# Optimization experiments

Hardware: AMD Instinct MI355X
Metric: run time of the kernel (lower is better)

The kernel has to match this reference:

```python
import jax, jax.numpy as jnp
import numpy as np

N, E, IN, HID, OUT = 8192, 262144, 3000, 256, 64
EPS = 1e-5


def setup_inputs() -> dict:
    key = jax.random.key(0)
    k = jax.random.split(key, 16)
    s = lambda i, shp, sc: jax.random.normal(k[i], shp, jnp.float32) * sc
    return {
        "feat": s(0, (N, IN), 1.0),
        "feat_a": s(1, (N, IN), 1.0),
        "graph_neigh": jax.random.uniform(k[2], (N, N), jnp.float32),
        "W1": s(3, (IN, HID), (1.0 / IN) ** 0.5),
        "att_src": s(4, (HID,), (1.0 / HID) ** 0.5),
        "att_dst": s(5, (HID,), (1.0 / HID) ** 0.5),
        "W2": s(6, (HID, OUT), (1.0 / HID) ** 0.5),
        "Wd1": s(7, (OUT, HID), (1.0 / OUT) ** 0.5),
        "bd1": jnp.zeros((HID,), jnp.float32),
        "gamma": jnp.ones((HID,), jnp.float32),
        "beta": jnp.zeros((HID,), jnp.float32),
        "Wd2": s(8, (HID, IN), (1.0 / HID) ** 0.5),
        "bd2": jnp.zeros((IN,), jnp.float32),
        "disc_W": s(9, (OUT, OUT), (1.0 / OUT) ** 0.5),
        "disc_b": jnp.zeros((), jnp.float32),
        "edge_index": jax.random.randint(k[10], (2, E), 0, N),
    }


def _gat_conv1(x, W1, att_src, att_dst, src, dst):
    # GATConv, heads=1, concat=False, no self-loops, no bias
    h = x @ W1                                    # [N, HID]
    a_src = h @ att_src                           # [N]
    a_dst = h @ att_dst                           # [N]
    e = jax.nn.leaky_relu(a_src[src] + a_dst[dst], 0.2)   # [E]
    m = jax.ops.segment_max(e, dst, num_segments=N)
    p = jnp.exp(e - m[dst])
    z = jax.ops.segment_sum(p, dst, num_segments=N)
    alpha = p / (z[dst] + 1e-16)                  # segment softmax over in-edges
    return jax.ops.segment_sum(alpha[:, None] * h[src], dst, num_segments=N)


def _encode(x, W1, att_src, att_dst, W2, src, dst):
    h1 = jax.nn.elu(_gat_conv1(x, W1, att_src, att_dst, src, dst))
    # conv2 is invoked with attention=False -> GraphST GATConv returns only lin(x) (heads=1 mean)
    return h1 @ W2


def _decoder(h, Wd1, bd1, gamma, beta, Wd2, bd2):
    z = h @ Wd1 + bd1
    mu = z.mean(0)
    var = z.var(0)  # biased, matches torch BN training normalization
    z = (z - mu) * jax.lax.rsqrt(var + EPS) * gamma + beta
    z = jax.nn.elu(z)
    return z @ Wd2 + bd2


def _readout(h, mask):
    vsum = mask @ h                               # [N, OUT]
    g = vsum / mask.sum(1, keepdims=True)
    g = g / jnp.clip(jnp.linalg.norm(g, axis=1, keepdims=True), 1e-12)
    return jax.nn.sigmoid(g)


def reference(feat, feat_a, graph_neigh, W1, att_src, att_dst, W2, Wd1, bd1,
              gamma, beta, Wd2, bd2, disc_W, disc_b, edge_index):
    src, dst = edge_index[0], edge_index[1]
    h2 = _encode(feat, W1, att_src, att_dst, W2, src, dst)
    h2_a = _encode(feat_a, W1, att_src, att_dst, W2, src, dst)
    h3 = _decoder(h2, Wd1, bd1, gamma, beta, Wd2, bd2)
    g = _readout(h2, graph_neigh)
    g_a = _readout(h2_a, graph_neigh)

    def disc(c, hp, hm):
        sc1 = jnp.einsum('nd,de,ne->n', hp, disc_W, c) + disc_b
        sc2 = jnp.einsum('nd,de,ne->n', hm, disc_W, c) + disc_b
        return jnp.stack([sc1, sc2], axis=1)

    ret = disc(g, h2, h2_a)
    ret_a = disc(g_a, h2_a, h2)
    return (h2, h3, ret, ret_a, h2, h2_a)
```

## Files before the change

kernel.cpp:

```cpp
#include <hip/hip_runtime.h>
#include <hip/hip_bf16.h>
#include <math.h>

constexpr int NN  = 8192;
constexpr int EE  = 262144;
constexpr int IN  = 3000;
constexpr int INP = 3008;
constexpr int HID = 256;
constexpr int OUT = 64;

constexpr long O_H2   = 0;
constexpr long O_H3   = 524288;
constexpr long O_RET  = 25100288;
constexpr long O_RETA = 25116672;
constexpr long O_H2B  = 25133056;
constexpr long O_H2A  = 25657344;

typedef __attribute__((ext_vector_type(8))) short short8v;
typedef __attribute__((ext_vector_type(4))) float f32x4;

__device__ __forceinline__ short f2bf(float f) {
    unsigned u = __float_as_uint(f);
    return (short)((u + 0x7FFF + ((u >> 16) & 1)) >> 16);
}
__device__ __forceinline__ float bf2f(unsigned short u) {
    return __uint_as_float(((unsigned)u) << 16);
}

__global__ void cvt_W1t(const float* __restrict__ W, unsigned short* __restrict__ Wt) {
    int i = blockIdx.x * 256 + threadIdx.x;
    int n = i / INP, k = i % INP;
    Wt[i] = (k < IN) ? (unsigned short)f2bf(W[(long)k * HID + n]) : 0;
}
__global__ void cvt_W2t(const float* __restrict__ W, unsigned short* __restrict__ Wt) {
    int i = blockIdx.x * 256 + threadIdx.x;
    int n = i / HID, k = i % HID;
    Wt[i] = (unsigned short)f2bf(W[(long)k * OUT + n]);
}
__global__ void cvt_Wd1t(const float* __restrict__ W, unsigned short* __restrict__ Wt) {
    int i = blockIdx.x * 256 + threadIdx.x;
    int n = i / OUT, k = i % OUT;
    Wt[i] = (unsigned short)f2bf(W[(long)k * HID + n]);
}
__global__ void cvt_Wd2t(const float* __restrict__ W, unsigned short* __restrict__ Wt) {
    int i = blockIdx.x * 256 + threadIdx.x;
    int n = i / HID, k = i % HID;
    Wt[i] = (n < IN) ? (unsigned short)f2bf(W[(long)k * IN + n]) : 0;
}
__global__ void cvt_f2b(const float* __restrict__ a, unsigned short* __restrict__ b) {
    int i = blockIdx.x * 256 + threadIdx.x;
    b[i] = (unsigned short)f2bf(a[i]);
}

template<int AF32>
__global__ __launch_bounds__(256) void mfma_gemm128(const void* __restrict__ Av,
                                                    const unsigned short* __restrict__ Bt,
                                                    const float* __restrict__ bias,
                                                    float* __restrict__ Cf,
                                                    float* __restrict__ Cpart,
                                                    int M, int N, int lda, int ldb, int aK,
                                                    int tilesPerChunk, int totalTiles) {
    __shared__ unsigned short As[128][72];
    __shared__ unsigned short Bs[128][72];
    int t = threadIdx.x, w = t >> 6, l = t & 63;
    int row0 = blockIdx.y * 128, col0 = blockIdx.x * 128;
    int sr = t >> 1, sh = (t & 1) * 32;
    int wm = (w >> 1) * 64, wn = (w & 1) * 64;
    int fr = l & 15, fq = l >> 4;
    int kbeg = blockIdx.z * tilesPerChunk * 64;
    int ktiles = min(tilesPerChunk, totalTiles - blockIdx.z * tilesPerChunk);

    const float*          Af = (const float*)Av;
    const unsigned short* Ab = (const unsigned short*)Av;
    const unsigned short* Bp = Bt + (long)(col0 + sr) * ldb + sh;

    float4  paf[8];
    short8v pab[4];
    short8v pb[4];

    auto loadA = [&](int k0) {
        if (AF32) {
            const float* Ar = Af + (long)(row0 + sr) * lda + k0 + sh;
            if (k0 + 64 <= aK) {
#pragma unroll
                for (int q = 0; q < 8; ++q) paf[q] = *reinterpret_cast<const float4*>(Ar + q * 4);
            } else {
#pragma unroll
                for (int q = 0; q < 8; ++q) {
                    float4 v;
                    int kb = k0 + sh + q * 4;
                    v.x = (kb + 0 < aK) ? Ar[q * 4 + 0] : 0.f;
                    v.y = (kb + 1 < aK) ? Ar[q * 4 + 1] : 0.f;
                    v.z = (kb + 2 < aK) ? Ar[q * 4 + 2] : 0.f;
                    v.w = (kb + 3 < aK) ? Ar[q * 4 + 3] : 0.f;
                    paf[q] = v;
                }
            }
        } else {
            const unsigned short* Ar = Ab + (long)(row0 + sr) * lda + k0 + sh;
#pragma unroll
            for (int q = 0; q < 4; ++q) pab[q] = *reinterpret_cast<const short8v*>(Ar + q * 8);
        }
    };
    auto loadB = [&](int k0) {
#pragma unroll
        for (int q = 0; q < 4; ++q) pb[q] = *reinterpret_cast<const short8v*>(Bp + k0 + q * 8);
    };

    loadA(kbeg);
    loadB(kbeg);

    f32x4 acc[4][4] = {};
    for (int tt = 0; tt < ktiles; ++tt) {
        if (AF32) {
#pragma unroll
            for (int q = 0; q < 4; ++q) {
                float4 v0 = paf[q * 2], v1 = paf[q * 2 + 1];
                short8v s;
                s[0]=f2bf(v0.x); s[1]=f2bf(v0.y); s[2]=f2bf(v0.z); s[3]=f2bf(v0.w);
                s[4]=f2bf(v1.x); s[5]=f2bf(v1.y); s[6]=f2bf(v1.z); s[7]=f2bf(v1.w);
                *reinterpret_cast<short8v*>(&As[sr][sh + q * 8]) = s;
            }
        } else {
#pragma unroll
            for (int q = 0; q < 4; ++q)
                *reinterpret_cast<short8v*>(&As[sr][sh + q * 8]) = pab[q];
        }
#pragma unroll
        for (int q = 0; q < 4; ++q)
            *reinterpret_cast<short8v*>(&Bs[sr][sh + q * 8]) = pb[q];
        __syncthreads();
        if (tt + 1 < ktiles) {
            int k0 = kbeg + (tt + 1) * 64;
            loadA(k0);
            loadB(k0);
        }
#pragma unroll
        for (int kk = 0; kk < 2; ++kk) {
            short8v fa[4], fb[4];
#pragma unroll
            for (int i = 0; i < 4; ++i)
                fa[i] = *reinterpret_cast<const short8v*>(&As[wm + i * 16 + fr][kk * 32 + fq * 8]);
#pragma unroll
            for (int j = 0; j < 4; ++j)
                fb[j] = *reinterpret_cast<const short8v*>(&Bs[wn + j * 16 + fr][kk * 32 + fq * 8]);
#pragma unroll
            for (int i = 0; i < 4; ++i)
#pragma unroll
                for (int j = 0; j < 4; ++j)
                    acc[i][j] = __builtin_amdgcn_mfma_f32_16x16x32_bf16(fa[i], fb[j], acc[i][j], 0, 0, 0);
        }
        __syncthreads();
    }
    int dc = l & 15;
#pragma unroll
    for (int i = 0; i < 4; ++i)
#pragma unroll
        for (int j = 0; j < 4; ++j) {
            int c = col0 + wn + j * 16 + dc;
            if (Cpart) {
#pragma unroll
                for (int q = 0; q < 4; ++q) {
                    int r = row0 + wm + i * 16 + fq * 4 + q;
                    Cpart[((long)blockIdx.z * M + r) * N + c] = acc[i][j][q];
                }
            } else if (c < N) {
                float bb = bias ? bias[c] : 0.f;
#pragma unroll
                for (int q = 0; q < 4; ++q) {
                    int r = row0 + wm + i * 16 + fq * 4 + q;
                    Cf[(long)r * N + c] = acc[i][j][q] + bb;
                }
            }
        }
}

__global__ void reduce_cvt(const float* __restrict__ p, unsigned short* __restrict__ hb) {
    int i4 = (blockIdx.x * 256 + threadIdx.x) * 4;
    float4 a = *reinterpret_cast<const float4*>(p + i4);
    float4 b = *reinterpret_cast<const float4*>(p + 2097152 + i4);
    ushort4 r;
    r.x = (unsigned short)f2bf(a.x + b.x);
    r.y = (unsigned short)f2bf(a.y + b.y);
    r.z = (unsigned short)f2bf(a.z + b.z);
    r.w = (unsigned short)f2bf(a.w + b.w);
    *reinterpret_cast<ushort4*>(hb + i4) = r;
}

__global__ __launch_bounds__(256) void mfma_gemm_bf(const unsigned short* __restrict__ A,
                                                    const unsigned short* __restrict__ Bt,
                                                    const float* __restrict__ bias,
                                                    float* __restrict__ C,
                                                    unsigned short* __restrict__ Cb,
                                                    int M, int N, int Kp) {
    __shared__ unsigned short As[64][72];
    __shared__ unsigned short Bs[64][72];
    int t = threadIdx.x, w = t >> 6, l = t & 63;
    int row0 = blockIdx.y * 64, col0 = blockIdx.x * 64;
    int srow = t >> 2, scol = (t & 3) * 16;
    const unsigned short* Ap = A  + (long)(row0 + srow) * Kp + scol;
    const unsigned short* Bp = Bt + (long)(col0 + srow) * Kp + scol;
    int wm = (w >> 1) * 32, wn = (w & 1) * 32;
    int fr = l & 15, fq = l >> 4;
    int nk = Kp >> 6;

    short8v a0r, a1r, b0r, b1r;
    a0r = *reinterpret_cast<const short8v*>(Ap);
    a1r = *reinterpret_cast<const short8v*>(Ap + 8);
    b0r = *reinterpret_cast<const short8v*>(Bp);
    b1r = *reinterpret_cast<const short8v*>(Bp + 8);

    f32x4 acc[2][2] = {};
    for (int tt = 0; tt < nk; ++tt) {
        *reinterpret_cast<short8v*>(&As[srow][scol])     = a0r;
        *reinterpret_cast<short8v*>(&As[srow][scol + 8]) = a1r;
        *reinterpret_cast<short8v*>(&Bs[srow][scol])     = b0r;
        *reinterpret_cast<short8v*>(&Bs[srow][scol + 8]) = b1r;
        __syncthreads();
        if (tt + 1 < nk) {
            const unsigned short* Ap2 = Ap + (tt + 1) * 64;
            const unsigned short* Bp2 = Bp + (tt + 1) * 64;
            a0r = *reinterpret_cast<const short8v*>(Ap2);
            a1r = *reinterpret_cast<const short8v*>(Ap2 + 8);
            b0r = *reinterpret_cast<const short8v*>(Bp2);
            b1r = *reinterpret_cast<const short8v*>(Bp2 + 8);
        }
#pragma unroll
        for (int kk = 0; kk < 2; ++kk) {
            short8v fa0 = *reinterpret_cast<const short8v*>(&As[wm + fr][kk * 32 + fq * 8]);
            short8v fa1 = *reinterpret_cast<const short8v*>(&As[wm + 16 + fr][kk * 32 + fq * 8]);
            short8v fb0 = *reinterpret_cast<const short8v*>(&Bs[wn + fr][kk * 32 + fq * 8]);
            short8v fb1 = *reinterpret_cast<const short8v*>(&Bs[wn + 16 + fr][kk * 32 + fq * 8]);
            acc[0][0] = __builtin_amdgcn_mfma_f32_16x16x32_bf16(fa0, fb0, acc[0][0], 0, 0, 0);
            acc[0][1] = __builtin_amdgcn_mfma_f32_16x16x32_bf16(fa0, fb1, acc[0][1], 0, 0, 0);
            acc[1][0] = __builtin_amdgcn_mfma_f32_16x16x32_bf16(fa1, fb0, acc[1][0], 0, 0, 0);
            acc[1][1] = __builtin_amdgcn_mfma_f32_16x16x32_bf16(fa1, fb1, acc[1][1], 0, 0, 0);
        }
        __syncthreads();
    }
    int dc = l & 15;
#pragma unroll
    for (int i = 0; i < 2; ++i)
#pragma unroll
        for (int j = 0; j < 2; ++j) {
            int c = col0 + wn + j * 16 + dc;
            if (c < N) {
                float bb = bias ? bias[c] : 0.f;
#pragma unroll
                for (int q = 0; q < 4; ++q) {
                    int r = row0 + wm + i * 16 + fq * 4 + q;
                    float v = acc[i][j][q] + bb;
                    long idx = (long)r * N + c;
                    if (C)  C[idx]  = v;
                    if (Cb) Cb[idx] = (unsigned short)f2bf(v);
                }
            }
        }
}

__global__ __launch_bounds__(256) void readout_mfma2(const float* __restrict__ gn,
                                                     const unsigned short* __restrict__ HT,
                                                     float* __restrict__ vsum_part,
                                                     float* __restrict__ rowsum_part) {
    __shared__ unsigned short As[64][72];
    __shared__ unsigned short Bs[128][72];
    __shared__ float rsacc[64][4];
    int t = threadIdx.x, w = t >> 6, l = t & 63;
    int row0 = blockIdx.x * 64;
    int kc = blockIdx.y, kbeg = kc * 2048;
    int asr = t >> 2, asc = (t & 3) * 16;
    int bsr = t >> 1, bsc = (t & 1) * 32;
    const float*          Ap = gn + (long)(row0 + asr) * NN + kbeg + asc;
    const unsigned short* Bp = HT + (long)bsr * NN + kbeg + bsc;
    int wm = (w >> 1) * 32, wn = (w & 1) * 64;
    int fr = l & 15, fq = l >> 4;

    float4  a4[4];
    short8v b8[4];
#pragma unroll
    for (int q = 0; q < 4; ++q) a4[q] = *reinterpret_cast<const float4*>(Ap + q * 4);
#pragma unroll
    for (int q = 0; q < 4; ++q) b8[q] = *reinterpret_cast<const short8v*>(Bp + q * 8);

    f32x4 acc[2][4] = {};
    float myrs = 0.f;
    for (int it = 0; it < 32; ++it) {
#pragma unroll
        for (int q = 0; q < 4; ++q) {
            float4 v = a4[q];
            ushort4 s;
            s.x = (unsigned short)f2bf(v.x);
            s.y = (unsigned short)f2bf(v.y);
            s.z = (unsigned short)f2bf(v.z);
            s.w = (unsigned short)f2bf(v.w);
            *reinterpret_cast<ushort4*>(&As[asr][asc + q * 4]) = s;
            myrs += v.x + v.y + v.z + v.w;
        }
#pragma unroll
        for (int q = 0; q < 4; ++q)
            *reinterpret_cast<short8v*>(&Bs[bsr][bsc + q * 8]) = b8[q];
        __syncthreads();
        if (it + 1 < 32) {
            const float*          Ap2 = Ap + (it + 1) * 64;
            const unsigned short* Bp2 = Bp + (it + 1) * 64;
#pragma unroll
            for (int q = 0; q < 4; ++q) a4[q] = *reinterpret_cast<const float4*>(Ap2 + q * 4);
#pragma unroll
            for (int q = 0; q < 4; ++q) b8[q] = *reinterpret_cast<const short8v*>(Bp2 + q * 8);
        }
#pragma unroll
        for (int kk = 0; kk < 2; ++kk) {
            short8v fa0 = *reinterpret_cast<const short8v*>(&As[wm + fr][kk * 32 + fq * 8]);
            short8v fa1 = *reinterpret_cast<const short8v*>(&As[wm + 16 + fr][kk * 32 + fq * 8]);
#pragma unroll
            for (int j = 0; j < 4; ++j) {
                short8v fb = *reinterpret_cast<const short8v*>(&Bs[wn + j * 16 + fr][kk * 32 + fq * 8]);
                acc[0][j] = __builtin_amdgcn_mfma_f32_16x16x32_bf16(fa0, fb, acc[0][j], 0, 0, 0);
                acc[1][j] = __builtin_amdgcn_mfma_f32_16x16x32_bf16(fa1, fb, acc[1][j], 0, 0, 0);
            }
        }
        __syncthreads();
    }
    rsacc[asr][t & 3] = myrs;
    __syncthreads();
    if (t < 64)
        rowsum_part[(long)kc * NN + row0 + t] =
            rsacc[t][0] + rsacc[t][1] + rsacc[t][2] + rsacc[t][3];
    int dc = l & 15;
#pragma unroll
    for (int i = 0; i < 2; ++i)
#pragma unroll
        for (int j = 0; j < 4; ++j) {
            int c = wn + j * 16 + dc;
#pragma unroll
            for (int q = 0; q < 4; ++q) {
                int r = row0 + wm + i * 16 + fq * 4 + q;
                vsum_part[((long)kc * NN + r) * 128 + c] = acc[i][j][q];
            }
        }
}

__global__ void deg_count(const int* __restrict__ dst, int* __restrict__ deg) {
    int i = blockIdx.x * 256 + threadIdx.x;
    if (i < EE) atomicAdd(&deg[dst[i]], 1);
}

__global__ __launch_bounds__(256) void scan_offsets(const int* __restrict__ deg,
                                                    int* __restrict__ off,
                                                    int* __restrict__ cursor) {
    __shared__ int part[256];
    int t = threadIdx.x;
    int base = t * 32;
    int local[32];
    int s = 0;
#pragma unroll
    for (int i = 0; i < 32; ++i) { local[i] = s; s += deg[base + i]; }
    part[t] = s;
    __syncthreads();
    for (int o2 = 1; o2 < 256; o2 <<= 1) {
        int v = (t >= o2) ? part[t - o2] : 0;
        __syncthreads();
        part[t] += v;
        __syncthreads();
    }
    int pre = (t == 0) ? 0 : part[t - 1];
#pragma unroll
    for (int i = 0; i < 32; ++i) {
        int v = pre + local[i];
        off[base + i] = v;
        cursor[base + i] = v;
    }
}

__global__ void scatter_edges(const int* __restrict__ src, const int* __restrict__ dst,
                              int* __restrict__ cursor, int* __restrict__ ssrc) {
    int i = blockIdx.x * 256 + threadIdx.x;
    if (i >= EE) return;
    int slot = atomicAdd(&cursor[dst[i]], 1);
    ssrc[slot] = src[i];
}

__global__ void attn_coeff_bf(const unsigned short* __restrict__ h,
                              const float* __restrict__ att_src,
                              const float* __restrict__ att_dst,
                              float* __restrict__ a_src, float* __restrict__ a_dst) {
    int wave = threadIdx.x >> 6, lane = threadIdx.x & 63;
    int n = blockIdx.x * 4 + wave;
    ushort4 hv = *reinterpret_cast<const ushort4*>(&h[(long)n * HID + lane * 4]);
    float4 vs = *reinterpret_cast<const float4*>(&att_src[lane * 4]);
    float4 vd = *reinterpret_cast<const float4*>(&att_dst[lane * 4]);
    float h0 = bf2f(hv.x), h1 = bf2f(hv.y), h2v = bf2f(hv.z), h3v = bf2f(hv.w);
    float s1 = h0 * vs.x + h1 * vs.y + h2v * vs.z + h3v * vs.w;
    float s2 = h0 * vd.x + h1 * vd.y + h2v * vd.z + h3v * vd.w;
#pragma unroll
    for (int off = 32; off > 0; off >>= 1) {
        s1 += __shfl_down(s1, off);
        s2 += __shfl_down(s2, off);
    }
    if (lane == 0) { a_src[n] = s1; a_dst[n] = s2; }
}

__global__ __launch_bounds__(256) void gat_gather(const int* __restrict__ ssrc,
                                                  const int* __restrict__ off,
                                                  const int* __restrict__ deg,
                                                  const float* __restrict__ asrc,
                                                  const float* __restrict__ adst,
                                                  const unsigned short* __restrict__ h,
                                                  unsigned short* __restrict__ gat) {
    int wv = threadIdx.x >> 6, lane = threadIdx.x & 63;
    int d = blockIdx.x * 4 + wv;
    int o = off[d], n = deg[d];
    float ad = adst[d];

    float m = -INFINITY;
    for (int j = lane; j < n; j += 64) {
        float e = asrc[ssrc[o + j]] + ad;
        e = e > 0.f ? e : 0.2f * e;
        m = fmaxf(m, e);
    }
#pragma unroll
    for (int t = 32; t; t >>= 1) m = fmaxf(m, __shfl_xor(m, t));
    float z = 0.f;
    for (int j = lane; j < n; j += 64) {
        float e = asrc[ssrc[o + j]] + ad;
        e = e > 0.f ? e : 0.2f * e;
        z += expf(e - m);
    }
#pragma unroll
    for (int t = 32; t; t >>= 1) z += __shfl_xor(z, t);
    float zinv = 1.0f / (z + 1e-16f);

    float4 acc = {0.f, 0.f, 0.f, 0.f};
    int j = 0;
    for (; j + 2 <= n; j += 2) {
        int s0 = ssrc[o + j], s1 = ssrc[o + j + 1];
        const ushort4 h0 = *reinterpret_cast<const ushort4*>(&h[(long)s0 * HID + lane * 4]);
        const ushort4 h1 = *reinterpret_cast<const ushort4*>(&h[(long)s1 * HID + lane * 4]);
        float e0 = asrc[s0] + ad; e0 = e0 > 0.f ? e0 : 0.2f * e0;
        float e1 = asrc[s1] + ad; e1 = e1 > 0.f ? e1 : 0.2f * e1;
        float a0 = expf(e0 - m) * zinv;
        float a1 = expf(e1 - m) * zinv;
        acc.x += a0 * bf2f(h0.x) + a1 * bf2f(h1.x);
        acc.y += a0 * bf2f(h0.y) + a1 * bf2f(h1.y);
        acc.z += a0 * bf2f(h0.z) + a1 * bf2f(h1.z);
        acc.w += a0 * bf2f(h0.w) + a1 * bf2f(h1.w);
    }
    if (j < n) {
        int s0 = ssrc[o + j];
        const ushort4 h0 = *reinterpret_cast<const ushort4*>(&h[(long)s0 * HID + lane * 4]);
        float e0 = asrc[s0] + ad; e0 = e0 > 0.f ? e0 : 0.2f * e0;
        float a0 = expf(e0 - m) * zinv;
        acc.x += a0 * bf2f(h0.x); acc.y += a0 * bf2f(h0.y);
        acc.z += a0 * bf2f(h0.z); acc.w += a0 * bf2f(h0.w);
    }
    ushort4 r;
    r.x = (unsigned short)f2bf(acc.x > 0.f ? acc.x : expm1f(acc.x));
    r.y = (unsigned short)f2bf(acc.y > 0.f ? acc.y : expm1f(acc.y));
    r.z = (unsigned short)f2bf(acc.z > 0.f ? acc.z : expm1f(acc.z));
    r.w = (unsigned short)f2bf(acc.w > 0.f ? acc.w : expm1f(acc.w));
    *reinterpret_cast<ushort4*>(&gat[(long)d * HID + lane * 4]) = r;
}

__global__ void bn_partial(const float* __restrict__ zd, float* __restrict__ s,
                           float* __restrict__ sq) {
    int t = threadIdx.x;
    float a = 0.f, b = 0.f;
    int r0 = blockIdx.x * 128;
    for (int r = r0; r < r0 + 128; ++r) {
        float v = zd[(long)r * HID + t];
        a += v;
        b += v * v;
    }
    atomicAdd(&s[t], a);
    atomicAdd(&sq[t], b);
}

__global__ void bn_finalize(const float* __restrict__ s, const float* __restrict__ sq,
                            const float* __restrict__ gamma, const float* __restrict__ beta,
                            float* __restrict__ scale, float* __restrict__ shift) {
    int t = threadIdx.x;
    float mean = s[t] / (float)NN;
    float var  = sq[t] / (float)NN - mean * mean;
    float sc   = gamma[t] * rsqrtf(var + 1e-5f);
    scale[t] = sc;
    shift[t] = beta[t] - mean * sc;
}

__global__ void bn_apply_elu_bf(const float* __restrict__ zd, const float* __restrict__ scale,
                                const float* __restrict__ shift, unsigned short* __restrict__ zb) {
    for (long i = (long)blockIdx.x * blockDim.x + threadIdx.x; i < (long)NN * HID;
         i += (long)gridDim.x * blockDim.x) {
        int c = (int)(i & 255);
        float v = zd[i] * scale[c] + shift[c];
        v = v > 0.f ? v : expm1f(v);
        zb[i] = (unsigned short)f2bf(v);
    }
}

__global__ void pack_hcatT(const float* __restrict__ h2, const float* __restrict__ h2a,
                           unsigned short* __restrict__ HT) {
    int c = blockIdx.x;
    int r = blockIdx.y * 256 + threadIdx.x;
    float v = (c < 64) ? h2[(long)r * 64 + c] : h2a[(long)r * 64 + (c - 64)];
    HT[(long)c * NN + r] = (unsigned short)f2bf(v);
}

__global__ void readout_norm2(const float* __restrict__ vsum_part,
                              const float* __restrict__ rowsum_part,
                              float* __restrict__ g, float* __restrict__ ga) {
    int r = blockIdx.x;
    int c = threadIdx.x;
    float v = 0.f;
#pragma unroll
    for (int kc = 0; kc < 4; ++kc)
        v += vsum_part[((long)kc * NN + r) * 128 + c];
    float rs = 0.f;
#pragma unroll
    for (int kc = 0; kc < 4; ++kc)
        rs += rowsum_part[(long)kc * NN + r];
    v /= rs;
    int w = c >> 6, lane = c & 63;
    float sq = v * v;
#pragma unroll
    for (int off = 32; off > 0; off >>= 1) sq += __shfl_xor(sq, off);
    float nrm = fmaxf(sqrtf(sq), 1e-12f);
    float out = 1.0f / (1.0f + expf(-(v / nrm)));
    (w == 0 ? g : ga)[(long)r * 64 + lane] = out;
}

__global__ void disc_kernel(const float* __restrict__ h2, const float* __restrict__ h2a,
                            const float* __restrict__ g, const float* __restrict__ ga,
                            const float* __restrict__ W, const float* __restrict__ b,
                            float* __restrict__ ret, float* __restrict__ reta) {
    int n = blockIdx.x;
    int w = threadIdx.x >> 6, lane = threadIdx.x & 63;
    const float* c = (w == 0) ? g : ga;
    float u = 0.f;
#pragma unroll 8
    for (int e = 0; e < 64; ++e) u += W[lane * 64 + e] * c[(long)n * 64 + e];
    float hp = ((w == 0) ? h2 : h2a)[(long)n * 64 + lane];
    float hm = ((w == 0) ? h2a : h2)[(long)n * 64 + lane];
    float t1 = hp * u, t2 = hm * u;
    for (int off = 32; off > 0; off >>= 1) {
        t1 += __shfl_xor(t1, off);
        t2 += __shfl_xor(t2, off);
    }
    if (lane == 0) {
        float bb = b[0];
        if (w == 0) { ret[n * 2] = t1 + bb;  ret[n * 2 + 1] = t2 + bb; }
        else        { reta[n * 2] = t1 + bb; reta[n * 2 + 1] = t2 + bb; }
    }
}

__global__ void copy_h2(const float* __restrict__ h2, const float* __restrict__ h2a,
                        float* __restrict__ out) {
    int i = blockIdx.x * 256 + threadIdx.x;
    float v = h2[i], va = h2a[i];
    out[O_H2 + i]  = v;
    out[O_H2B + i] = v;
    out[O_H2A + i] = va;
}

extern "C" void kernel_launch(void* const* d_in, const int* in_sizes, int n_in,
                              void* d_out, int out_size, void* d_ws, size_t ws_size,
                              hipStream_t stream) {
    const float* feat    = (const float*)d_in[0];
    const float* feat_a  = (const float*)d_in[1];
    const float* gneigh  = (const float*)d_in[2];
    const float* W1      = (const float*)d_in[3];
    const float* att_src = (const float*)d_in[4];
    const float* att_dst = (const float*)d_in[5];
    const float* W2      = (const float*)d_in[6];
    const float* Wd1     = (const float*)d_in[7];
    const float* bd1     = (const float*)d_in[8];
    const float* gamma   = (const float*)d_in[9];
    const float* beta    = (const float*)d_in[10];
    const float* Wd2     = (const float*)d_in[11];
    const float* bd2     = (const float*)d_in[12];
    const float* disc_W  = (const float*)d_in[13];
    const float* disc_b  = (const float*)d_in[14];
    const int*   eidx    = (const int*)d_in[15];
    const int*   src = eidx;
    const int*   dst = eidx + EE;
    float* out = (float*)d_out;

    float* w = (float*)d_ws;
    float* h_buf   = w;
    unsigned short* h_bf = (unsigned short*)h_buf;
    unsigned short* gat_bf = (unsigned short*)(h_buf + 2097152);
    float* zdec    = h_buf + 2097152 + 1048576;
    unsigned short* zdec_bf = (unsigned short*)(zdec + 2097152);
    float* h2      = zdec + 2097152 + 1048576;
    float* h2a     = h2 + 524288;
    float* gbuf    = h2a + 524288;
    float* gabuf   = gbuf + 524288;
    unsigned short* h2b = (unsigned short*)(gabuf + 524288);
    float* asrc    = gabuf + 524288 + 262144;
    float* adst    = asrc + 8192;
    float* bnsum   = adst + 8192;
    float* bnsq    = bnsum + 256;
    float* scale   = bnsq + 256;
    float* shift   = scale + 256;
    unsigned short* W1t  = (unsigned short*)(shift + 256);
    unsigned short* W2t  = W1t + 770048;
    unsigned short* Wd1t = W2t + 16384;
    unsigned short* Wd2t = Wd1t + 16384;
    int*   ideg    = (int*)(Wd2t + 786432);
    int*   ioff    = ideg + 8192;
    int*   icur    = ioff + 8192;
    int*   issrc   = icur + 8192;
    float* part = w + 2097152;
    float* vsum_part = h_buf;
    unsigned short* HT = zdec_bf;
    float* rowsum_part = ((float*)zdec_bf) + 524288;

    cvt_W1t<<<3008, 256, 0, stream>>>(W1, W1t);
    cvt_W2t<<<64, 256, 0, stream>>>(W2, W2t);
    cvt_Wd1t<<<64, 256, 0, stream>>>(Wd1, Wd1t);
    cvt_Wd2t<<<3072, 256, 0, stream>>>(Wd2, Wd2t);

    hipMemsetAsync(ideg, 0, 8192 * 4, stream);
    deg_count<<<EE / 256, 256, 0, stream>>>(dst, ideg);
    scan_offsets<<<1, 256, 0, stream>>>(ideg, ioff, icur);
    scatter_edges<<<EE / 256, 256, 0, stream>>>(src, dst, icur, issrc);

    auto encode_pass = [&](const float* x, float* h2_out) {
        mfma_gemm128<1><<<dim3(2, 64, 2), 256, 0, stream>>>(
            x, W1t, nullptr, nullptr, part, NN, HID, IN, INP, IN, 24, 47);
        reduce_cvt<<<2048, 256, 0, stream>>>(part, h_bf);
        attn_coeff_bf<<<2048, 256, 0, stream>>>(h_bf, att_src, att_dst, asrc, adst);
        gat_gather<<<2048, 256, 0, stream>>>(issrc, ioff, ideg, asrc, adst, h_bf, gat_bf);
        mfma_gemm_bf<<<dim3(1, 128), 256, 0, stream>>>(gat_bf, W2t, nullptr,
                                                       h2_out, h2b, NN, OUT, HID);
    };

    encode_pass(feat, h2);
    encode_pass(feat_a, h2a);
    cvt_f2b<<<2048, 256, 0, stream>>>(h2, h2b);

    mfma_gemm_bf<<<dim3(4, 128), 256, 0, stream>>>(h2b, Wd1t, bd1,
                                                   zdec, nullptr, NN, HID, OUT);
    hipMemsetAsync(bnsum, 0, 512 * 4, stream);
    bn_partial<<<64, 256, 0, stream>>>(zdec, bnsum, bnsq);
    bn_finalize<<<1, 256, 0, stream>>>(bnsum, bnsq, gamma, beta, scale, shift);
    bn_apply_elu_bf<<<2048, 256, 0, stream>>>(zdec, scale, shift, zdec_bf);
    mfma_gemm128<0><<<dim3(24, 64, 1), 256, 0, stream>>>(
        zdec_bf, Wd2t, bd2, out + O_H3, nullptr, NN, IN, HID, HID, HID, 4, 4);

    pack_hcatT<<<dim3(128, 32), 256, 0, stream>>>(h2, h2a, HT);
    readout_mfma2<<<dim3(128, 4), 256, 0, stream>>>(gneigh, HT, vsum_part, rowsum_part);
    readout_norm2<<<8192, 128, 0, stream>>>(vsum_part, rowsum_part, gbuf, gabuf);

    disc_kernel<<<8192, 128, 0, stream>>>(h2, h2a, gbuf, gabuf, disc_W, disc_b,
                                          out + O_RET, out + O_RETA);

    copy_h2<<<2048, 256, 0, stream>>>(h2, h2a, out);
}
```

Measured before the change: 449.8 us.

## Batch both encoder passes into single launches and fuse epilogues and readout kernels

Both encoder passes (feat and feat_a) now run in one launch each for the W1 GEMM, attention coefficients, GAT gather and W2 GEMM. The split-K partial buffer and its reduce kernel are gone: the W1 GEMM runs over the full K and writes bf16 directly. The W2 GEMM epilogue also writes the fp32 outputs, the bf16 copy and the transposed readout operand, which removes the cvt, pack and copy kernels. Readout normalization and the discriminator are merged into one kernel. This cuts launches and intermediate memory traffic, but the W1 GEMM drops from 256 blocks of 24 K-tiles to 256 blocks of 47 K-tiles, so each block runs a longer serial K loop.

```diff
diff --git a/kernel.cpp b/kernel.cpp
--- a/kernel.cpp
+++ b/kernel.cpp
@@ -47,94 +47,67 @@
     int n = i / HID, k = i % HID;
     Wt[i] = (n < IN) ? (unsigned short)f2bf(W[(long)k * IN + n]) : 0;
 }
-__global__ void cvt_f2b(const float* __restrict__ a, unsigned short* __restrict__ b) {
-    int i = blockIdx.x * 256 + threadIdx.x;
-    b[i] = (unsigned short)f2bf(a[i]);
-}
-
-template<int AF32>
-__global__ __launch_bounds__(256) void mfma_gemm128(const void* __restrict__ Av,
-                                                    const unsigned short* __restrict__ Bt,
-                                                    const float* __restrict__ bias,
-                                                    float* __restrict__ Cf,
-                                                    float* __restrict__ Cpart,
-                                                    int M, int N, int lda, int ldb, int aK,
-                                                    int tilesPerChunk, int totalTiles) {
+
+__global__ __launch_bounds__(256) void feat_gemm(const float* __restrict__ A0,
+                                                 const float* __restrict__ A1,
+                                                 const unsigned short* __restrict__ Bt,
+                                                 unsigned short* __restrict__ Hb) {
     __shared__ unsigned short As[128][72];
     __shared__ unsigned short Bs[128][72];
+    int id = blockIdx.x;
+    int xb = id >> 7, yb = id & 127;
+    int pass = yb >> 6;
+    int row0 = (yb & 63) * 128, col0 = xb * 128;
+    const float* A = pass ? A1 : A0;
     int t = threadIdx.x, w = t >> 6, l = t & 63;
-    int row0 = blockIdx.y * 128, col0 = blockIdx.x * 128;
     int sr = t >> 1, sh = (t & 1) * 32;
     int wm = (w >> 1) * 64, wn = (w & 1) * 64;
     int fr = l & 15, fq = l >> 4;
-    int kbeg = blockIdx.z * tilesPerChunk * 64;
-    int ktiles = min(tilesPerChunk, totalTiles - blockIdx.z * tilesPerChunk);
-
-    const float*          Af = (const float*)Av;
-    const unsigned short* Ab = (const unsigned short*)Av;
-    const unsigned short* Bp = Bt + (long)(col0 + sr) * ldb + sh;
+    const unsigned short* Bp = Bt + (long)(col0 + sr) * INP + sh;
+    const float* Arow = A + (long)(row0 + sr) * IN;
 
     float4  paf[8];
-    short8v pab[4];
     short8v pb[4];
-
     auto loadA = [&](int k0) {
-        if (AF32) {
-            const float* Ar = Af + (long)(row0 + sr) * lda + k0 + sh;
-            if (k0 + 64 <= aK) {
-#pragma unroll
-                for (int q = 0; q < 8; ++q) paf[q] = *reinterpret_cast<const float4*>(Ar + q * 4);
-            } else {
-#pragma unroll
-                for (int q = 0; q < 8; ++q) {
-                    float4 v;
-                    int kb = k0 + sh + q * 4;
-                    v.x = (kb + 0 < aK) ? Ar[q * 4 + 0] : 0.f;
-                    v.y = (kb + 1 < aK) ? Ar[q * 4 + 1] : 0.f;
-                    v.z = (kb + 2 < aK) ? Ar[q * 4 + 2] : 0.f;
-                    v.w = (kb + 3 < aK) ? Ar[q * 4 + 3] : 0.f;
-                    paf[q] = v;
-                }
+        const float* Ar = Arow + k0 + sh;
+        if (k0 + 64 <= IN) {
+#pragma unroll
+            for (int q = 0; q < 8; ++q) paf[q] = *reinterpret_cast<const float4*>(Ar + q * 4);
+        } else {
+#pragma unroll
+            for (int q = 0; q < 8; ++q) {
+                int kb = k0 + sh + q * 4;
+                float4 v;
+                v.x = (kb + 0 < IN) ? Ar[q * 4 + 0] : 0.f;
+                v.y = (kb + 1 < IN) ? Ar[q * 4 + 1] : 0.f;
+                v.z = (kb + 2 < IN) ? Ar[q * 4 + 2] : 0.f;
+                v.w = (kb + 3 < IN) ? Ar[q * 4 + 3] : 0.f;
+                paf[q] = v;
             }
-        } else {
-            const unsigned short* Ar = Ab + (long)(row0 + sr) * lda + k0 + sh;
-#pragma unroll
-            for (int q = 0; q < 4; ++q) pab[q] = *reinterpret_cast<const short8v*>(Ar + q * 8);
         }
     };
     auto loadB = [&](int k0) {
 #pragma unroll
         for (int q = 0; q < 4; ++q) pb[q] = *reinterpret_cast<const short8v*>(Bp + k0 + q * 8);
     };
-
-    loadA(kbeg);
-    loadB(kbeg);
-
+    loadA(0); loadB(0);
+
+    constexpr int NK = INP / 64;
     f32x4 acc[4][4] = {};
-    for (int tt = 0; tt < ktiles; ++tt) {
-        if (AF32) {
-#pragma unroll
-            for (int q = 0; q < 4; ++q) {
-                float4 v0 = paf[q * 2], v1 = paf[q * 2 + 1];
-                short8v s;
-                s[0]=f2bf(v0.x); s[1]=f2bf(v0.y); s[2]=f2bf(v0.z); s[3]=f2bf(v0.w);
-                s[4]=f2bf(v1.x); s[5]=f2bf(v1.y); s[6]=f2bf(v1.z); s[7]=f2bf(v1.w);
-                *reinterpret_cast<short8v*>(&As[sr][sh + q * 8]) = s;
-            }
-        } else {
-#pragma unroll
-            for (int q = 0; q < 4; ++q)
-                *reinterpret_cast<short8v*>(&As[sr][sh + q * 8]) = pab[q];
+    for (int tt = 0; tt < NK; ++tt) {
+#pragma unroll
+        for (int q = 0; q < 4; ++q) {
+            float4 v0 = paf[q * 2], v1 = paf[q * 2 + 1];
+            short8v s;
+            s[0]=f2bf(v0.x); s[1]=f2bf(v0.y); s[2]=f2bf(v0.z); s[3]=f2bf(v0.w);
+            s[4]=f2bf(v1.x); s[5]=f2bf(v1.y); s[6]=f2bf(v1.z); s[7]=f2bf(v1.w);
+            *reinterpret_cast<short8v*>(&As[sr][sh + q * 8]) = s;
         }
 #pragma unroll
         for (int q = 0; q < 4; ++q)
             *reinterpret_cast<short8v*>(&Bs[sr][sh + q * 8]) = pb[q];
         __syncthreads();
-        if (tt + 1 < ktiles) {
-            int k0 = kbeg + (tt + 1) * 64;
-            loadA(k0);
-            loadB(k0);
-        }
+        if (tt + 1 < NK) { loadA((tt + 1) * 64); loadB((tt + 1) * 64); }
 #pragma unroll
         for (int kk = 0; kk < 2; ++kk) {
             short8v fa[4], fb[4];
@@ -153,56 +126,35 @@
         __syncthreads();
     }
     int dc = l & 15;
+    long base = (long)(pass * NN) * HID;
 #pragma unroll
     for (int i = 0; i < 4; ++i)
 #pragma unroll
         for (int j = 0; j < 4; ++j) {
             int c = col0 + wn + j * 16 + dc;
-            if (Cpart) {
-#pragma unroll
-                for (int q = 0; q < 4; ++q) {
-                    int r = row0 + wm + i * 16 + fq * 4 + q;
-                    Cpart[((long)blockIdx.z * M + r) * N + c] = acc[i][j][q];
-                }
-            } else if (c < N) {
-                float bb = bias ? bias[c] : 0.f;
-#pragma unroll
-                for (int q = 0; q < 4; ++q) {
-                    int r = row0 + wm + i * 16 + fq * 4 + q;
-                    Cf[(long)r * N + c] = acc[i][j][q] + bb;
-                }
+#pragma unroll
+            for (int q = 0; q < 4; ++q) {
+                int r = row0 + wm + i * 16 + fq * 4 + q;
+                Hb[base + (long)r * HID + c] = (unsigned short)f2bf(acc[i][j][q]);
             }
         }
 }
 
-__global__ void reduce_cvt(const float* __restrict__ p, unsigned short* __restrict__ hb) {
-    int i4 = (blockIdx.x * 256 + threadIdx.x) * 4;
-    float4 a = *reinterpret_cast<const float4*>(p + i4);
-    float4 b = *reinterpret_cast<const float4*>(p + 2097152 + i4);
-    ushort4 r;
-    r.x = (unsigned short)f2bf(a.x + b.x);
-    r.y = (unsigned short)f2bf(a.y + b.y);
-    r.z = (unsigned short)f2bf(a.z + b.z);
-    r.w = (unsigned short)f2bf(a.w + b.w);
-    *reinterpret_cast<ushort4*>(hb + i4) = r;
-}
-
-__global__ __launch_bounds__(256) void mfma_gemm_bf(const unsigned short* __restrict__ A,
-                                                    const unsigned short* __restrict__ Bt,
-                                                    const float* __restrict__ bias,
-                                                    float* __restrict__ C,
-                                                    unsigned short* __restrict__ Cb,
-                                                    int M, int N, int Kp) {
+__global__ __launch_bounds__(256) void w2_gemm(const unsigned short* __restrict__ A,
+                                               const unsigned short* __restrict__ Bt,
+                                               float* __restrict__ h2f,
+                                               unsigned short* __restrict__ h2b,
+                                               unsigned short* __restrict__ HT,
+                                               float* __restrict__ out) {
     __shared__ unsigned short As[64][72];
     __shared__ unsigned short Bs[64][72];
     int t = threadIdx.x, w = t >> 6, l = t & 63;
-    int row0 = blockIdx.y * 64, col0 = blockIdx.x * 64;
+    int row0 = blockIdx.y * 64;
     int srow = t >> 2, scol = (t & 3) * 16;
-    const unsigned short* Ap = A  + (long)(row0 + srow) * Kp + scol;
-    const unsigned short* Bp = Bt + (long)(col0 + srow) * Kp + scol;
+    const unsigned short* Ap = A + (long)(row0 + srow) * HID + scol;
+    const unsigned short* Bp = Bt + (long)srow * HID + scol;
     int wm = (w >> 1) * 32, wn = (w & 1) * 32;
     int fr = l & 15, fq = l >> 4;
-    int nk = Kp >> 6;
 
     short8v a0r, a1r, b0r, b1r;
     a0r = *reinterpret_cast<const short8v*>(Ap);
@@ -211,13 +163,13 @@
     b1r = *reinterpret_cast<const short8v*>(Bp + 8);
 
     f32x4 acc[2][2] = {};
-    for (int tt = 0; tt < nk; ++tt) {
+    for (int tt = 0; tt < 4; ++tt) {
         *reinterpret_cast<short8v*>(&As[srow][scol])     = a0r;
         *reinterpret_cast<short8v*>(&As[srow][scol + 8]) = a1r;
         *reinterpret_cast<short8v*>(&Bs[srow][scol])     = b0r;
         *reinterpret_cast<short8v*>(&Bs[srow][scol + 8]) = b1r;
         __syncthreads();
-        if (tt + 1 < nk) {
+        if (tt + 1 < 4) {
             const unsigned short* Ap2 = Ap + (tt + 1) * 64;
             const unsigned short* Bp2 = Bp + (tt + 1) * 64;
             a0r = *reinterpret_cast<const short8v*>(Ap2);
@@ -239,21 +191,142 @@
         __syncthreads();
     }
     int dc = l & 15;
+    int pass = row0 >> 13;
+#pragma unroll
+    for (int i = 0; i < 2; ++i)
+#pragma unroll
+        for (int j = 0; j < 2; ++j) {
+            int c = wn + j * 16 + dc;
+#pragma unroll
+            for (int q = 0; q < 4; ++q) {
+                int r = row0 + wm + i * 16 + fq * 4 + q;
+                int n = r & 8191;
+                float v = acc[i][j][q];
+                unsigned short vb = (unsigned short)f2bf(v);
+                h2f[(long)pass * 524288 + (long)n * 64 + c] = v;
+                if (pass == 0) {
+                    out[O_H2  + (long)n * 64 + c] = v;
+                    out[O_H2B + (long)n * 64 + c] = v;
+                    h2b[(long)n * 64 + c] = vb;
+                } else {
+                    out[O_H2A + (long)n * 64 + c] = v;
+                }
+                HT[(long)(pass * 64 + c) * NN + n] = vb;
+            }
+        }
+}
+
+__global__ __launch_bounds__(256) void wd2_gemm(const unsigned short* __restrict__ A,
+                                                const unsigned short* __restrict__ Bt,
+                                                const float* __restrict__ bias,
+                                                float* __restrict__ Cf) {
+    __shared__ unsigned short As[128][72];
+    __shared__ unsigned short Bs[128][72];
+    int t = threadIdx.x, w = t >> 6, l = t & 63;
+    int row0 = blockIdx.y * 128, col0 = blockIdx.x * 128;
+    int sr = t >> 1, sh = (t & 1) * 32;
+    int wm = (w >> 1) * 64, wn = (w & 1) * 64;
+    int fr = l & 15, fq = l >> 4;
+    const unsigned short* Ap = A  + (long)(row0 + sr) * HID + sh;
+    const unsigned short* Bp = Bt + (long)(col0 + sr) * HID + sh;
+
+    short8v pa[4], pb[4];
+#pragma unroll
+    for (int q = 0; q < 4; ++q) pa[q] = *reinterpret_cast<const short8v*>(Ap + q * 8);
+#pragma unroll
+    for (int q = 0; q < 4; ++q) pb[q] = *reinterpret_cast<const short8v*>(Bp + q * 8);
+
+    f32x4 acc[4][4] = {};
+    for (int tt = 0; tt < 4; ++tt) {
+#pragma unroll
+        for (int q = 0; q < 4; ++q) {
+            *reinterpret_cast<short8v*>(&As[sr][sh + q * 8]) = pa[q];
+            *reinterpret_cast<short8v*>(&Bs[sr][sh + q * 8]) = pb[q];
+        }
+        __syncthreads();
+        if (tt + 1 < 4) {
+            int k0 = (tt + 1) * 64;
+#pragma unroll
+            for (int q = 0; q < 4; ++q) pa[q] = *reinterpret_cast<const short8v*>(Ap + k0 + q * 8);
+#pragma unroll
+            for (int q = 0; q < 4; ++q) pb[q] = *reinterpret_cast<const short8v*>(Bp + k0 + q * 8);
+        }
+#pragma unroll
+        for (int kk = 0; kk < 2; ++kk) {
+            short8v fa[4], fb[4];
+#pragma unroll
+            for (int i = 0; i < 4; ++i)
+                fa[i] = *reinterpret_cast<const short8v*>(&As[wm + i * 16 + fr][kk * 32 + fq * 8]);
+#pragma unroll
+            for (int j = 0; j < 4; ++j)
+                fb[j] = *reinterpret_cast<const short8v*>(&Bs[wn + j * 16 + fr][kk * 32 + fq * 8]);
+#pragma unroll
+            for (int i = 0; i < 4; ++i)
+#pragma unroll
+                for (int j = 0; j < 4; ++j)
+                    acc[i][j] = __builtin_amdgcn_mfma_f32_16x16x32_bf16(fa[i], fb[j], acc[i][j], 0, 0, 0);
+        }
+        __syncthreads();
+    }
+    int dc = l & 15;
+#pragma unroll
+    for (int i = 0; i < 4; ++i)
+#pragma unroll
+        for (int j = 0; j < 4; ++j) {
+            int c = col0 + wn + j * 16 + dc;
+            if (c < IN) {
+                float bb = bias[c];
+#pragma unroll
+                for (int q = 0; q < 4; ++q) {
+                    int r = row0 + wm + i * 16 + fq * 4 + q;
+                    Cf[(long)r * IN + c] = acc[i][j][q] + bb;
+                }
+            }
+        }
+}
+
+__global__ __launch_bounds__(256) void wd1_gemm(const unsigned short* __restrict__ A,
+                                                const unsigned short* __restrict__ Bt,
+                                                const float* __restrict__ bias,
+                                                float* __restrict__ C) {
+    __shared__ unsigned short As[64][72];
+    __shared__ unsigned short Bs[64][72];
+    int t = threadIdx.x, w = t >> 6, l = t & 63;
+    int row0 = blockIdx.y * 64, col0 = blockIdx.x * 64;
+    int srow = t >> 2, scol = (t & 3) * 16;
+    const unsigned short* Ap = A  + (long)(row0 + srow) * OUT + scol;
+    const unsigned short* Bp = Bt + (long)(col0 + srow) * OUT + scol;
+    int wm = (w >> 1) * 32, wn = (w & 1) * 32;
+    int fr = l & 15, fq = l >> 4;
+
+    *reinterpret_cast<short8v*>(&As[srow][scol])     = *reinterpret_cast<const short8v*>(Ap);
+    *reinterpret_cast<short8v*>(&As[srow][scol + 8]) = *reinterpret_cast<const short8v*>(Ap + 8);
+    *reinterpret_cast<short8v*>(&Bs[srow][scol])     = *reinterpret_cast<const short8v*>(Bp);
+    *reinterpret_cast<short8v*>(&Bs[srow][scol + 8]) = *reinterpret_cast<const short8v*>(Bp + 8);
+    __syncthreads();
+    f32x4 acc[2][2] = {};
+#pragma unroll
+    for (int kk = 0; kk < 2; ++kk) {
+        short8v fa0 = *reinterpret_cast<const short8v*>(&As[wm + fr][kk * 32 + fq * 8]);
+        short8v fa1 = *reinterpret_cast<const short8v*>(&As[wm + 16 + fr][kk * 32 + fq * 8]);
+        short8v fb0 = *reinterpret_cast<const short8v*>(&Bs[wn + fr][kk * 32 + fq * 8]);
+        short8v fb1 = *reinterpret_cast<const short8v*>(&Bs[wn + 16 + fr][kk * 32 + fq * 8]);
+        acc[0][0] = __builtin_amdgcn_mfma_f32_16x16x32_bf16(fa0, fb0, acc[0][0], 0, 0, 0);
+        acc[0][1] = __builtin_amdgcn_mfma_f32_16x16x32_bf16(fa0, fb1, acc[0][1], 0, 0, 0);
+        acc[1][0] = __builtin_amdgcn_mfma_f32_16x16x32_bf16(fa1, fb0, acc[1][0], 0, 0, 0);
+        acc[1][1] = __builtin_amdgcn_mfma_f32_16x16x32_bf16(fa1, fb1, acc[1][1], 0, 0, 0);
+    }
+    int dc = l & 15;
 #pragma unroll
     for (int i = 0; i < 2; ++i)
 #pragma unroll
         for (int j = 0; j < 2; ++j) {
             int c = col0 + wn + j * 16 + dc;
-            if (c < N) {
-                float bb = bias ? bias[c] : 0.f;
-#pragma unroll
-                for (int q = 0; q < 4; ++q) {
-                    int r = row0 + wm + i * 16 + fq * 4 + q;
-                    float v = acc[i][j][q] + bb;
-                    long idx = (long)r * N + c;
-                    if (C)  C[idx]  = v;
-                    if (Cb) Cb[idx] = (unsigned short)f2bf(v);
-                }
+            float bb = bias[c];
+#pragma unroll
+            for (int q = 0; q < 4; ++q) {
+                int r = row0 + wm + i * 16 + fq * 4 + q;
+                C[(long)r * HID + c] = acc[i][j][q] + bb;
             }
         }
 }
@@ -403,14 +476,17 @@
 __global__ __launch_bounds__(256) void gat_gather(const int* __restrict__ ssrc,
                                                   const int* __restrict__ off,
                                                   const int* __restrict__ deg,
-                                                  const float* __restrict__ asrc,
-                                                  const float* __restrict__ adst,
-                                                  const unsigned short* __restrict__ h,
-                                                  unsigned short* __restrict__ gat) {
+                                                  const float* __restrict__ asrc2,
+                                                  const float* __restrict__ adst2,
+                                                  const unsigned short* __restrict__ hb2,
+                                                  unsigned short* __restrict__ gat2) {
     int wv = threadIdx.x >> 6, lane = threadIdx.x & 63;
     int d = blockIdx.x * 4 + wv;
-    int o = off[d], n = deg[d];
-    float ad = adst[d];
+    int pass = d >> 13, node = d & 8191;
+    const float* asrc = asrc2 + pass * NN;
+    const unsigned short* h = hb2 + (long)pass * NN * HID;
+    int o = off[node], n = deg[node];
+    float ad = adst2[d];
 
     float m = -INFINITY;
     for (int j = lane; j < n; j += 64) {
@@ -458,7 +534,7 @@
     r.y = (unsigned short)f2bf(acc.y > 0.f ? acc.y : expm1f(acc.y));
     r.z = (unsigned short)f2bf(acc.z > 0.f ? acc.z : expm1f(acc.z));
     r.w = (unsigned short)f2bf(acc.w > 0.f ? acc.w : expm1f(acc.w));
-    *reinterpret_cast<ushort4*>(&gat[(long)d * HID + lane * 4]) = r;
+    *reinterpret_cast<ushort4*>(&gat2[(long)d * HID + lane * 4]) = r;
 }
 
 __global__ void bn_partial(const float* __restrict__ zd, float* __restrict__ s,
@@ -497,68 +573,46 @@
     }
 }
 
-__global__ void pack_hcatT(const float* __restrict__ h2, const float* __restrict__ h2a,
-                           unsigned short* __restrict__ HT) {
-    int c = blockIdx.x;
-    int r = blockIdx.y * 256 + threadIdx.x;
-    float v = (c < 64) ? h2[(long)r * 64 + c] : h2a[(long)r * 64 + (c - 64)];
-    HT[(long)c * NN + r] = (unsigned short)f2bf(v);
-}
-
-__global__ void readout_norm2(const float* __restrict__ vsum_part,
-                              const float* __restrict__ rowsum_part,
-                              float* __restrict__ g, float* __restrict__ ga) {
-    int r = blockIdx.x;
-    int c = threadIdx.x;
-    float v = 0.f;
-#pragma unroll
-    for (int kc = 0; kc < 4; ++kc)
-        v += vsum_part[((long)kc * NN + r) * 128 + c];
-    float rs = 0.f;
-#pragma unroll
-    for (int kc = 0; kc < 4; ++kc)
+__global__ void readout_disc(const float* __restrict__ vsum_part,
+                             const float* __restrict__ rowsum_part,
+                             const float* __restrict__ h2f,
+                             const float* __restrict__ W, const float* __restrict__ b,
+                             float* __restrict__ ret, float* __restrict__ reta) {
+    __shared__ float gg[128];
+    int r = blockIdx.x, t = threadIdx.x;
+    float rs = 0.f, v = 0.f;
+#pragma unroll
+    for (int kc = 0; kc < 4; ++kc) {
         rs += rowsum_part[(long)kc * NN + r];
+        v  += vsum_part[((long)kc * NN + r) * 128 + t];
+    }
     v /= rs;
-    int w = c >> 6, lane = c & 63;
+    int w = t >> 6, lane = t & 63;
     float sq = v * v;
 #pragma unroll
     for (int off = 32; off > 0; off >>= 1) sq += __shfl_xor(sq, off);
     float nrm = fmaxf(sqrtf(sq), 1e-12f);
-    float out = 1.0f / (1.0f + expf(-(v / nrm)));
-    (w == 0 ? g : ga)[(long)r * 64 + lane] = out;
-}
-
-__global__ void disc_kernel(const float* __restrict__ h2, const float* __restrict__ h2a,
-                            const float* __restrict__ g, const float* __restrict__ ga,
-                            const float* __restrict__ W, const float* __restrict__ b,
-                            float* __restrict__ ret, float* __restrict__ reta) {
-    int n = blockIdx.x;
-    int w = threadIdx.x >> 6, lane = threadIdx.x & 63;
-    const float* c = (w == 0) ? g : ga;
+    gg[t] = 1.0f / (1.0f + expf(-(v / nrm)));
+    __syncthreads();
+    const float* hp_base = h2f + (w ? 524288 : 0);
+    const float* hm_base = h2f + (w ? 0 : 524288);
     float u = 0.f;
 #pragma unroll 8
-    for (int e = 0; e < 64; ++e) u += W[lane * 64 + e] * c[(long)n * 64 + e];
-    float hp = ((w == 0) ? h2 : h2a)[(long)n * 64 + lane];
-    float hm = ((w == 0) ? h2a : h2)[(long)n * 64 + lane];
+    for (int e = 0; e < 64; ++e) u += W[lane * 64 + e] * gg[w * 64 + e];
+    float hp = hp_base[(long)r * 64 + lane];
+    float hm = hm_base[(long)r * 64 + lane];
     float t1 = hp * u, t2 = hm * u;
+#pragma unroll
     for (int off = 32; off > 0; off >>= 1) {
         t1 += __shfl_xor(t1, off);
         t2 += __shfl_xor(t2, off);
     }
     if (lane == 0) {
         float bb = b[0];
-        if (w == 0) { ret[n * 2] = t1 + bb;  ret[n * 2 + 1] = t2 + bb; }
-        else        { reta[n * 2] = t1 + bb; reta[n * 2 + 1] = t2 + bb; }
-    }
-}
-
-__global__ void copy_h2(const float* __restrict__ h2, const float* __restrict__ h2a,
-                        float* __restrict__ out) {
-    int i = blockIdx.x * 256 + threadIdx.x;
-    float v = h2[i], va = h2a[i];
-    out[O_H2 + i]  = v;
-    out[O_H2B + i] = v;
-    out[O_H2A + i] = va;
+        float* dstp = w ? reta : ret;
+        dstp[r * 2]     = t1 + bb;
+        dstp[r * 2 + 1] = t2 + bb;
+    }
 }
 
 extern "C" void kernel_launch(void* const* d_in, const int* in_sizes, int n_in,
@@ -585,19 +639,16 @@
     float* out = (float*)d_out;
 
     float* w = (float*)d_ws;
-    float* h_buf   = w;
-    unsigned short* h_bf = (unsigned short*)h_buf;
-    unsigned short* gat_bf = (unsigned short*)(h_buf + 2097152);
-    float* zdec    = h_buf + 2097152 + 1048576;
+    unsigned short* h_bf2  = (unsigned short*)w;
+    unsigned short* gat_bf2 = (unsigned short*)(w + 2097152);
+    float* zdec    = w + 4194304;
     unsigned short* zdec_bf = (unsigned short*)(zdec + 2097152);
-    float* h2      = zdec + 2097152 + 1048576;
-    float* h2a     = h2 + 524288;
-    float* gbuf    = h2a + 524288;
-    float* gabuf   = gbuf + 524288;
-    unsigned short* h2b = (unsigned short*)(gabuf + 524288);
-    float* asrc    = gabuf + 524288 + 262144;
-    float* adst    = asrc + 8192;
-    float* bnsum   = adst + 8192;
+    float* h2f     = zdec + 2097152 + 1048576;
+    unsigned short* h2b = (unsigned short*)(h2f + 1048576);
+    unsigned short* HT  = h2b + 524288;
+    float* asrc2   = (float*)(HT + 1048576);
+    float* adst2   = asrc2 + 16384;
+    float* bnsum   = adst2 + 16384;
     float* bnsq    = bnsum + 256;
     float* scale   = bnsq + 256;
     float* shift   = scale + 256;
@@ -609,10 +660,8 @@
     int*   ioff    = ideg + 8192;
     int*   icur    = ioff + 8192;
     int*   issrc   = icur + 8192;
-    float* part = w + 2097152;
-    float* vsum_part = h_buf;
-    unsigned short* HT = zdec_bf;
-    float* rowsum_part = ((float*)zdec_bf) + 524288;
+    float* vsum_part = w;
+    float* rowsum_part = zdec;
 
     cvt_W1t<<<3008, 256, 0, stream>>>(W1, W1t);
     cvt_W2t<<<64, 256, 0, stream>>>(W2, W2t);
@@ -624,35 +673,19 @@
     scan_offsets<<<1, 256, 0, stream>>>(ideg, ioff, icur);
     scatter_edges<<<EE / 256, 256, 0, stream>>>(src, dst, icur, issrc);
 
-    auto encode_pass = [&](const float* x, float* h2_out) {
-        mfma_gemm128<1><<<dim3(2, 64, 2), 256, 0, stream>>>(
-            x, W1t, nullptr, nullptr, part, NN, HID, IN, INP, IN, 24, 47);
-        reduce_cvt<<<2048, 256, 0, stream>>>(part, h_bf);
-        attn_coeff_bf<<<2048, 256, 0, stream>>>(h_bf, att_src, att_dst, asrc, adst);
-        gat_gather<<<2048, 256, 0, stream>>>(issrc, ioff, ideg, asrc, adst, h_bf, gat_bf);
-        mfma_gemm_bf<<<dim3(1, 128), 256, 0, stream>>>(gat_bf, W2t, nullptr,
-                                                       h2_out, h2b, NN, OUT, HID);
-    };
-
-    encode_pass(feat, h2);
-    encode_pass(feat_a, h2a);
-    cvt_f2b<<<2048, 256, 0, stream>>>(h2, h2b);
-
-    mfma_gemm_bf<<<dim3(4, 128), 256, 0, stream>>>(h2b, Wd1t, bd1,
-                                                   zdec, nullptr, NN, HID, OUT);
+    feat_gemm<<<256, 256, 0, stream>>>(feat, feat_a, W1t, h_bf2);
+    attn_coeff_bf<<<4096, 256, 0, stream>>>(h_bf2, att_src, att_dst, asrc2, adst2);
+    gat_gather<<<4096, 256, 0, stream>>>(issrc, ioff, ideg, asrc2, adst2, h_bf2, gat_bf2);
+    w2_gemm<<<dim3(1, 256), 256, 0, stream>>>(gat_bf2, W2t, h2f, h2b, HT, out);
+
+    wd1_gemm<<<dim3(4, 128), 256, 0, stream>>>(h2b, Wd1t, bd1, zdec);
     hipMemsetAsync(bnsum, 0, 512 * 4, stream);
     bn_partial<<<64, 256, 0, stream>>>(zdec, bnsum, bnsq);
     bn_finalize<<<1, 256, 0, stream>>>(bnsum, bnsq, gamma, beta, scale, shift);
     bn_apply_elu_bf<<<2048, 256, 0, stream>>>(zdec, scale, shift, zdec_bf);
-    mfma_gemm128<0><<<dim3(24, 64, 1), 256, 0, stream>>>(
-        zdec_bf, Wd2t, bd2, out + O_H3, nullptr, NN, IN, HID, HID, HID, 4, 4);
-
-    pack_hcatT<<<dim3(128, 32), 256, 0, stream>>>(h2, h2a, HT);
+    wd2_gemm<<<dim3(24, 64), 256, 0, stream>>>(zdec_bf, Wd2t, bd2, out + O_H3);
+
     readout_mfma2<<<dim3(128, 4), 256, 0, stream>>>(gneigh, HT, vsum_part, rowsum_part);
-    readout_norm2<<<8192, 128, 0, stream>>>(vsum_part, rowsum_part, gbuf, gabuf);
-
-    disc_kernel<<<8192, 128, 0, stream>>>(h2, h2a, gbuf, gabuf, disc_W, disc_b,
-                                          out + O_RET, out + O_RETA);
-
-    copy_h2<<<2048, 256, 0, stream>>>(h2, h2a, out);
-}
+    readout_disc<<<8192, 128, 0, stream>>>(vsum_part, rowsum_part, h2f, disc_W, disc_b,
+                                           out + O_RET, out + O_RETA);
+}
```

Result: faster. 419.5 us (-6.7%).
